# Kernel tuning notes

Measured on AMD Instinct MI355X. Metric: run time of the kernel, lower is better.

Reference implementation:

```python
import jax, jax.numpy as jnp
import numpy as np

ALPHA = 0.5  # trapezoidal_alpha

def rmsnorm(x, w, eps=1e-5):
    return x * jax.lax.rsqrt(jnp.mean(x * x, axis=-1, keepdims=True) + eps) * w

def ssd_scan(x, Bc, Cc, dt, A, alpha):
    # x: (B,L,H,P), Bc/Cc: (B,L,N), dt: (B,L,H), A: (H,)
    da = jnp.exp(dt * A)  # (B,L,H), A < 0 so da in (0,1)
    shift = lambda t: jnp.concatenate([jnp.zeros_like(t[:, :1]), t[:, :-1]], axis=1)
    xp, bp, dtp = shift(x), shift(Bc), shift(dt)
    to_t = lambda t: jnp.moveaxis(t, 1, 0)
    xs = tuple(map(to_t, (x, Bc, Cc, dt, da, xp, bp, dtp)))
    Bb, _, H, P = x.shape
    N = Bc.shape[-1]
    h0 = jnp.zeros((Bb, H, P, N), x.dtype)
    def step(h, inp):
        xt, bt, ct, dtt, dat, xpt, bpt, dtpt = inp
        u = dtt[:, :, None, None] * xt[..., None] * bt[:, None, None, :]      # (B,H,P,N)
        up = dtpt[:, :, None, None] * xpt[..., None] * bpt[:, None, None, :]  # prev input term
        h = dat[:, :, None, None] * (h + alpha * up) + (1.0 - alpha) * u      # trapezoidal update
        y = jnp.einsum('bhpn,bn->bhp', h, ct)
        return h, y
    _, ys = jax.lax.scan(step, h0, xs)
    return jnp.moveaxis(ys, 0, 1)  # (B,L,H,P)

def setup_inputs() -> dict:
    key = jax.random.key(0)
    ks = jax.random.split(key, 10)
    B, NV, NQ = 4, 256, 32
    D, DI, H, N, E, NL = 1024, 2048, 32, 128, 1536, 12
    PROJ = 2 * DI + 2 * N + H  # z | x | B | C | dt
    s = 0.02
    return {
        'visual_tokens': jax.random.normal(ks[0], (B, NV, D), jnp.float32),
        'query_embeds': jax.random.normal(ks[1], (B, NQ, D), jnp.float32),
        'vis_w': jax.random.normal(ks[2], (D, D), jnp.float32) * s,
        'vis_b': jnp.zeros((D,), jnp.float32),
        'qry_w': jax.random.normal(ks[3], (D, D), jnp.float32) * s,
        'qry_b': jnp.zeros((D,), jnp.float32),
        'norm_ws': jnp.ones((NL, D), jnp.float32),
        'in_ws': jax.random.normal(ks[4], (NL, D, PROJ), jnp.float32) * s,
        'dt_biases': jax.random.normal(ks[5], (NL, H), jnp.float32) * 0.5,
        'A_logs': jnp.log(jnp.tile(jnp.arange(1.0, H + 1.0, dtype=jnp.float32)[None], (NL, 1))),
        'D_ssm': jnp.ones((NL, H), jnp.float32),
        'gnorm_ws': jnp.ones((NL, DI), jnp.float32),
        'out_ws': jax.random.normal(ks[6], (NL, DI, D), jnp.float32) * s,
        'norm_f_w': jnp.ones((D,), jnp.float32),
        'head_w': jax.random.normal(ks[7], (D, E), jnp.float32) * s,
        'head_b': jnp.zeros((E,), jnp.float32),
    }

def reference(visual_tokens, query_embeds, vis_w, vis_b, qry_w, qry_b, norm_ws, in_ws,
              dt_biases, A_logs, D_ssm, gnorm_ws, out_ws, norm_f_w, head_w, head_b):
    vis = visual_tokens @ vis_w + vis_b
    qry = query_embeds @ qry_w + qry_b
    hidden = jnp.concatenate([vis, qry], axis=1)  # (B,L,D)
    n_layers = in_ws.shape[0]
    d_inner = gnorm_ws.shape[-1]
    H = A_logs.shape[-1]
    P = d_inner // H
    N = (in_ws.shape[-1] - 2 * d_inner - H) // 2
    for i in range(n_layers):
        res = hidden
        xin = rmsnorm(hidden, norm_ws[i])
        proj = xin @ in_ws[i]  # (B,L,2*DI+2*N+H)
        z = proj[..., :d_inner]
        xss = proj[..., d_inner:2 * d_inner]
        Bc = proj[..., 2 * d_inner:2 * d_inner + N]
        Cc = proj[..., 2 * d_inner + N:2 * d_inner + 2 * N]
        dt = jax.nn.softplus(proj[..., 2 * d_inner + 2 * N:] + dt_biases[i])
        A = -jnp.exp(A_logs[i])
        xr = xss.reshape(xss.shape[0], xss.shape[1], H, P)
        y = ssd_scan(xr, Bc, Cc, dt, A, ALPHA) + D_ssm[i][None, None, :, None] * xr
        y = y.reshape(xss.shape)
        y = rmsnorm(y * jax.nn.silu(z), gnorm_ws[i])  # gated RMSNorm
        hidden = res + y @ out_ws[i]
    hidden = rmsnorm(hidden, norm_f_w)
    pooled = hidden.mean(axis=1)                   # (B,D)
    out = pooled @ head_w + head_b                 # (B,E)
    nrm = jnp.linalg.norm(out, axis=-1, keepdims=True)
    return out / jnp.maximum(nrm, 1e-12)           # F.normalize semantics
```

## Files before the change

kernel.cpp:

```cpp
#include <hip/hip_runtime.h>
#include <cmath>

#define Bb   4
#define Tt   288
#define Dd   1024
#define DIi  2048
#define HH   32
#define PP   64
#define NNs  128
#define PROJ  4384
#define PROJP 4480
#define NLl  12
#define EE   1536

typedef __bf16 bf16x8 __attribute__((ext_vector_type(8)));
typedef float f32x4 __attribute__((ext_vector_type(4)));
typedef float f32x16 __attribute__((ext_vector_type(16)));

__device__ __forceinline__ unsigned short f2bf(float v) {
  __bf16 b = (__bf16)v;
  return __builtin_bit_cast(unsigned short, b);
}
__device__ __forceinline__ float bf2f(unsigned short u) {
  unsigned int x = ((unsigned int)u) << 16;
  return __builtin_bit_cast(float, x);
}
__device__ __forceinline__ void split2(float v, unsigned short& h, unsigned short& l) {
  h = f2bf(v);
  l = f2bf(v - bf2f(h));
}

__device__ __forceinline__ void async16(const void* g, void* l) {
  __builtin_amdgcn_global_load_lds(
      (const __attribute__((address_space(1))) unsigned int*)g,
      (__attribute__((address_space(3))) unsigned int*)l, 16, 0, 0);
}

__device__ inline float block_reduce_sum(float v, float* lds) {
#pragma unroll
  for (int d = 32; d > 0; d >>= 1) v += __shfl_down(v, d, 64);
  int lane = threadIdx.x & 63;
  int w = threadIdx.x >> 6;
  if (lane == 0) lds[w] = v;
  __syncthreads();
  if (threadIdx.x == 0) {
    float s = lds[0];
    int nw = blockDim.x >> 6;
    for (int i = 1; i < nw; i++) s += lds[i];
    lds[0] = s;
  }
  __syncthreads();
  return lds[0];
}

__global__ __launch_bounds__(256) void cvt_act_k(const float* __restrict__ vis,
                                                 const float* __restrict__ qry,
                                                 unsigned short* __restrict__ oh,
                                                 unsigned short* __restrict__ ol) {
  int idx = (blockIdx.x * 256 + threadIdx.x) * 4;
  const float* src = (idx < 1024 * 1024) ? &vis[idx] : &qry[idx - 1024 * 1024];
  float4 v = *(const float4*)src;
  ushort4 h, l;
  split2(v.x, h.x, l.x); split2(v.y, h.y, l.y);
  split2(v.z, h.z, l.z); split2(v.w, h.w, l.w);
  *(ushort4*)&oh[idx] = h;
  *(ushort4*)&ol[idx] = l;
}

__global__ __launch_bounds__(256) void cvt_tr2_k(const float* __restrict__ W,
                                                 unsigned short* __restrict__ Wth,
                                                 unsigned short* __restrict__ Wtl,
                                                 int K, int N,
                                                 size_t wstride, size_t ostride) {
  __shared__ float tile[32][33];
  W   += (size_t)blockIdx.z * wstride;
  Wth += (size_t)blockIdx.z * ostride;
  Wtl += (size_t)blockIdx.z * ostride;
  const int n0 = blockIdx.x * 32, k0 = blockIdx.y * 32;
  const int c = threadIdx.x & 31;
  const int r0 = threadIdx.x >> 5;
#pragma unroll
  for (int j = 0; j < 4; j++) {
    int r = r0 + j * 8;
    int n = n0 + c;
    tile[r][c] = (n < N) ? W[(size_t)(k0 + r) * N + n] : 0.f;
  }
  __syncthreads();
  const int nl = threadIdx.x >> 3;
  const int kl = (threadIdx.x & 7) * 4;
  ushort4 h, l;
  split2(tile[kl + 0][nl], h.x, l.x);
  split2(tile[kl + 1][nl], h.y, l.y);
  split2(tile[kl + 2][nl], h.z, l.z);
  split2(tile[kl + 3][nl], h.w, l.w);
  size_t o = (size_t)(n0 + nl) * K + k0 + kl;
  *(ushort4*)&Wth[o] = h;
  *(ushort4*)&Wtl[o] = l;
}

template<int BM, int BN>
__global__ __launch_bounds__(256) void gemm3_k(
    const unsigned short* __restrict__ Ah, const unsigned short* __restrict__ Al,
    const unsigned short* __restrict__ Wh, const unsigned short* __restrict__ Wl,
    const float* __restrict__ bias, const float* __restrict__ res,
    float* __restrict__ C, int M, int N, int K,
    int rows_per_b, int T_total, int t_off)
{
  constexpr int FM = BM / 64;
  constexpr int FN = BN / 64;
  __shared__ __align__(16) unsigned short Ash[BM * 32];
  __shared__ __align__(16) unsigned short Asl[BM * 32];
  __shared__ __align__(16) unsigned short Bsh[BN * 32];
  __shared__ __align__(16) unsigned short Bsl[BN * 32];
  const int tid = threadIdx.x;
  const int lane = tid & 63;
  const int wm = (tid >> 6) >> 1;
  const int wn = (tid >> 6) & 1;
  const int m0 = blockIdx.y * BM;
  const int n0 = blockIdx.x * BN;
  const int lrow = lane & 31;
  const int lkb = (lane >> 5) * 8;

  f32x16 acc[FM][FN];
#pragma unroll
  for (int i = 0; i < FM; i++)
#pragma unroll
    for (int j = 0; j < FN; j++) acc[i][j] = (f32x16)0.0f;

  for (int k0 = 0; k0 < K; k0 += 32) {
#pragma unroll
    for (int c = 0; c < BM / 64; c++) {
      int o = (c * 256 + tid) * 16;
      int row = o >> 6;
      int colb = o & 63;
      size_t gb = ((size_t)(m0 + row) * K + k0) * 2 + colb;
      async16((const char*)Ah + gb, (char*)Ash + o);
      async16((const char*)Al + gb, (char*)Asl + o);
    }
#pragma unroll
    for (int c = 0; c < BN / 64; c++) {
      int o = (c * 256 + tid) * 16;
      int row = o >> 6;
      int colb = o & 63;
      size_t gb = ((size_t)(n0 + row) * K + k0) * 2 + colb;
      async16((const char*)Wh + gb, (char*)Bsh + o);
      async16((const char*)Wl + gb, (char*)Bsl + o);
    }
    __syncthreads();

#pragma unroll
    for (int kh = 0; kh < 2; kh++) {
      bf16x8 ah[FM], al[FM], bh[FN], bl[FN];
#pragma unroll
      for (int i = 0; i < FM; i++) {
        int off = (wm * (BM / 2) + i * 32 + lrow) * 32 + kh * 16 + lkb;
        ah[i] = *(const bf16x8*)&Ash[off];
        al[i] = *(const bf16x8*)&Asl[off];
      }
#pragma unroll
      for (int j = 0; j < FN; j++) {
        int off = (wn * (BN / 2) + j * 32 + lrow) * 32 + kh * 16 + lkb;
        bh[j] = *(const bf16x8*)&Bsh[off];
        bl[j] = *(const bf16x8*)&Bsl[off];
      }
#pragma unroll
      for (int i = 0; i < FM; i++)
#pragma unroll
        for (int j = 0; j < FN; j++) {
          acc[i][j] = __builtin_amdgcn_mfma_f32_32x32x16_bf16(ah[i], bh[j], acc[i][j], 0, 0, 0);
          acc[i][j] = __builtin_amdgcn_mfma_f32_32x32x16_bf16(ah[i], bl[j], acc[i][j], 0, 0, 0);
          acc[i][j] = __builtin_amdgcn_mfma_f32_32x32x16_bf16(al[i], bh[j], acc[i][j], 0, 0, 0);
        }
    }
    __syncthreads();
  }

  const int r0 = (lane >> 5) * 4;
#pragma unroll
  for (int i = 0; i < FM; i++) {
#pragma unroll
    for (int j = 0; j < FN; j++) {
      int ncol = n0 + wn * (BN / 2) + j * 32 + lrow;
      float bv = bias ? bias[ncol] : 0.f;
#pragma unroll
      for (int rg = 0; rg < 16; rg++) {
        int m = m0 + wm * (BM / 2) + i * 32 + (rg & 3) + 8 * (rg >> 2) + r0;
        size_t orow;
        if (T_total) {
          int bbv = m / rows_per_b;
          orow = (size_t)bbv * T_total + (m - bbv * rows_per_b) + t_off;
        } else {
          orow = (size_t)m;
        }
        float v = acc[i][j][rg] + bv;
        if (res) v += res[orow * N + ncol];
        C[orow * N + ncol] = v;
      }
    }
  }
}

__global__ __launch_bounds__(256) void gemm_k(
    const float* __restrict__ A, const float* __restrict__ W,
    const float* __restrict__ bias, const float* __restrict__ res,
    float* __restrict__ C, int M, int N, int K,
    int rows_per_b, int T_total, int t_off)
{
  __shared__ float As[16][64];
  __shared__ float Ws[16][64];
  const int tid = threadIdx.x;
  const int tx = tid & 15;
  const int ty = tid >> 4;
  const int m0 = blockIdx.y * 64;
  const int n0 = blockIdx.x * 64;
  float acc[4][4] = {};
  const int ar = tid >> 2;
  const int ac = (tid & 3) << 2;
  const int wr = tid >> 4;
  const int wc = (tid & 15) << 2;

  for (int k0 = 0; k0 < K; k0 += 16) {
    float4 av = {0.f, 0.f, 0.f, 0.f};
    int gr = m0 + ar;
    if (gr < M) av = *(const float4*)&A[(size_t)gr * K + k0 + ac];
    As[ac + 0][ar] = av.x; As[ac + 1][ar] = av.y;
    As[ac + 2][ar] = av.z; As[ac + 3][ar] = av.w;

    float4 wv = {0.f, 0.f, 0.f, 0.f};
    int gc = n0 + wc;
    const float* wp = &W[(size_t)(k0 + wr) * N + gc];
    if (gc + 3 < N) {
      wv = *(const float4*)wp;
    } else {
      if (gc + 0 < N) wv.x = wp[0];
      if (gc + 1 < N) wv.y = wp[1];
      if (gc + 2 < N) wv.z = wp[2];
    }
    *(float4*)&Ws[wr][wc] = wv;
    __syncthreads();
#pragma unroll
    for (int kk = 0; kk < 16; kk++) {
      float4 a4 = *(const float4*)&As[kk][ty << 2];
      float4 b4 = *(const float4*)&Ws[kk][tx << 2];
      float a[4] = {a4.x, a4.y, a4.z, a4.w};
      float b[4] = {b4.x, b4.y, b4.z, b4.w};
#pragma unroll
      for (int i = 0; i < 4; i++)
#pragma unroll
        for (int j = 0; j < 4; j++)
          acc[i][j] = fmaf(a[i], b[j], acc[i][j]);
    }
    __syncthreads();
  }
#pragma unroll
  for (int i = 0; i < 4; i++) {
    int gr = m0 + (ty << 2) + i;
    if (gr >= M) continue;
    int bbv = gr / rows_per_b;
    int tt = gr - bbv * rows_per_b;
    size_t orow = (size_t)bbv * T_total + tt + t_off;
#pragma unroll
    for (int j = 0; j < 4; j++) {
      int gc = n0 + (tx << 2) + j;
      if (gc >= N) continue;
      float v = acc[i][j];
      if (bias) v += bias[gc];
      if (res)  v += res[orow * (size_t)N + gc];
      C[orow * (size_t)N + gc] = v;
    }
  }
}

__global__ __launch_bounds__(256) void rmsnorm_k(
    const float* __restrict__ x, const float* __restrict__ w, float* __restrict__ out)
{
  __shared__ float lds[8];
  const int row = blockIdx.x;
  const float* xr = x + (size_t)row * Dd;
  float4 v = *(const float4*)&xr[threadIdx.x << 2];
  float ss = v.x * v.x + v.y * v.y + v.z * v.z + v.w * v.w;
  ss = block_reduce_sum(ss, lds);
  float sc = rsqrtf(ss * (1.f / Dd) + 1e-5f);
  float4 wv = *(const float4*)&w[threadIdx.x << 2];
  float4 o = {v.x * sc * wv.x, v.y * sc * wv.y, v.z * sc * wv.z, v.w * sc * wv.w};
  *(float4*)&out[(size_t)row * Dd + (threadIdx.x << 2)] = o;
}

__global__ __launch_bounds__(256) void rmsnorm2_k(
    const float* __restrict__ x, const float* __restrict__ w,
    unsigned short* __restrict__ oh, unsigned short* __restrict__ ol)
{
  __shared__ float lds[8];
  const int row = blockIdx.x;
  const float* xr = x + (size_t)row * Dd;
  float4 v = *(const float4*)&xr[threadIdx.x << 2];
  float ss = v.x * v.x + v.y * v.y + v.z * v.z + v.w * v.w;
  ss = block_reduce_sum(ss, lds);
  float sc = rsqrtf(ss * (1.f / Dd) + 1e-5f);
  float4 wv = *(const float4*)&w[threadIdx.x << 2];
  ushort4 h, l;
  split2(v.x * sc * wv.x, h.x, l.x);
  split2(v.y * sc * wv.y, h.y, l.y);
  split2(v.z * sc * wv.z, h.z, l.z);
  split2(v.w * sc * wv.w, h.w, l.w);
  size_t o = (size_t)row * Dd + (threadIdx.x << 2);
  *(ushort4*)&oh[o] = h;
  *(ushort4*)&ol[o] = l;
}

__global__ __launch_bounds__(64) void dtcum_k(
    const float* __restrict__ proj, const float* __restrict__ dt_bias,
    const float* __restrict__ A_log,
    float* __restrict__ dtt, double* __restrict__ dcum)
{
  const int h = blockIdx.x & 31;
  const int b = blockIdx.x >> 5;
  const int lane = threadIdx.x;
  const float A = -expf(A_log[h]);
  const float bias = dt_bias[h];
  const int rowo = (b * HH + h) * Tt;
  double base = 0.0;
  for (int c = 0; c < (Tt + 63) / 64; c++) {
    int t = c * 64 + lane;
    float dt = 0.f;
    if (t < Tt) {
      float v = proj[(size_t)(b * Tt + t) * PROJP + 2 * DIi + 2 * NNs + h] + bias;
      dt = (v > 20.f) ? v : log1pf(expf(v));
    }
    double a = (double)(dt * A);
#pragma unroll
    for (int d = 1; d < 64; d <<= 1) {
      double o = __shfl_up(a, d, 64);
      if (lane >= d) a += o;
    }
    double cum = base + a;
    if (t < Tt) { dtt[rowo + t] = dt; dcum[rowo + t] = cum; }
    base = __shfl(cum, 63, 64);
  }
}

__global__ __launch_bounds__(256) void cbgemm_k(const float* __restrict__ proj,
                                                float* __restrict__ St)
{
  const int tI = blockIdx.x, jI = blockIdx.y, b = blockIdx.z;
  if (jI > tI) return;
  __shared__ float Ct[32][130];
  __shared__ float Bt[32][130];
  const int tid = threadIdx.x;
  const int r = tid >> 3;
  const int q = (tid & 7) * 16;
  const float* pb = proj + (size_t)b * Tt * PROJP;
  {
    const float* crow = pb + (size_t)(tI * 32 + r) * PROJP + 2 * DIi + NNs + q;
    const float* brow = pb + (size_t)(jI * 32 + r) * PROJP + 2 * DIi + q;
#pragma unroll
    for (int f = 0; f < 16; f += 4) {
      float4 c4 = *(const float4*)&crow[f];
      float4 b4 = *(const float4*)&brow[f];
      *(float2*)&Ct[r][q + f]     = make_float2(c4.x, c4.y);
      *(float2*)&Ct[r][q + f + 2] = make_float2(c4.z, c4.w);
      *(float2*)&Bt[r][q + f]     = make_float2(b4.x, b4.y);
      *(float2*)&Bt[r][q + f + 2] = make_float2(b4.z, b4.w);
    }
  }
  __syncthreads();
  const int j_r = tid >> 3;
  const int t_c = (tid & 7) * 4;
  float acc[4] = {0.f, 0.f, 0.f, 0.f};
  for (int n = 0; n < NNs; n += 2) {
    float2 b2 = *(const float2*)&Bt[j_r][n];
#pragma unroll
    for (int k = 0; k < 4; k++) {
      float2 c2 = *(const float2*)&Ct[t_c + k][n];
      acc[k] = fmaf(b2.x, c2.x, acc[k]);
      acc[k] = fmaf(b2.y, c2.y, acc[k]);
    }
  }
  float* so = St + ((size_t)b * Tt + jI * 32 + j_r) * Tt + tI * 32 + t_c;
  *(float4*)so = make_float4(acc[0], acc[1], acc[2], acc[3]);
}

__global__ __launch_bounds__(256) void ssd_y_k(
    const float* __restrict__ proj, const float* __restrict__ St,
    const float* __restrict__ dtt, const double* __restrict__ dcum,
    const float* __restrict__ Dssm, float* __restrict__ ybuf)
{
  const int tI = blockIdx.x;
  const int h  = blockIdx.y;
  const int b  = blockIdx.z;
  __shared__ __align__(16) float Xs[32][64];
  __shared__ __align__(16) float Ss[32][36];
  __shared__ double cjs[32];
  const int tid = threadIdx.x;
  const int t_l = tid & 31;
  const int pg  = tid >> 5;
  const int t0  = tI * 32;
  const int rowo = (b * HH + h) * Tt;
  const double ct = dcum[rowo + t0 + t_l];
  const float Ds = Dssm[h];
  const float* pb = proj + (size_t)b * Tt * PROJP;
  float y[8] = {0,0,0,0,0,0,0,0};
  const int sr = tid >> 3;
  const int sq = tid & 7;

  for (int jI = 0; jI <= tI; jI++) {
    const int j0 = jI * 32;
    {
      const float* xr = pb + (size_t)(j0 + sr) * PROJP + DIi + h * PP + sq * 8;
      *(float4*)&Xs[sr][sq * 8]     = *(const float4*)&xr[0];
      *(float4*)&Xs[sr][sq * 8 + 4] = *(const float4*)&xr[4];
    }
    {
      const float* srow = St + ((size_t)b * Tt + j0 + sr) * Tt + t0 + sq * 4;
      float4 s4 = *(const float4*)srow;
      float dj = dtt[rowo + j0 + sr];
      s4.x *= dj; s4.y *= dj; s4.z *= dj; s4.w *= dj;
      *(float4*)&Ss[sr][sq * 4] = s4;
    }
    if (tid < 32) cjs[tid] = dcum[rowo + j0 + tid];
    __syncthreads();

    if (jI < tI) {
#pragma unroll 4
      for (int j = 0; j < 32; j++) {
        float d = (float)(ct - cjs[j]);
        float m = Ss[j][t_l] * expf(fminf(d, 0.f));
        const float* xp = &Xs[j][pg * 8];
        float4 a0 = *(const float4*)&xp[0];
        float4 a1 = *(const float4*)&xp[4];
        y[0] = fmaf(m, a0.x, y[0]); y[1] = fmaf(m, a0.y, y[1]);
        y[2] = fmaf(m, a0.z, y[2]); y[3] = fmaf(m, a0.w, y[3]);
        y[4] = fmaf(m, a1.x, y[4]); y[5] = fmaf(m, a1.y, y[5]);
        y[6] = fmaf(m, a1.z, y[6]); y[7] = fmaf(m, a1.w, y[7]);
      }
    } else {
      for (int j = 0; j < 32; j++) {
        float sv = Ss[j][t_l];
        float d = (float)(ct - cjs[j]);
        float m = sv * expf(fminf(d, 0.f));
        if (j == t_l) m = 0.5f * sv + Ds;
        if (j > t_l)  m = 0.f;
        const float* xp = &Xs[j][pg * 8];
        float4 a0 = *(const float4*)&xp[0];
        float4 a1 = *(const float4*)&xp[4];
        y[0] = fmaf(m, a0.x, y[0]); y[1] = fmaf(m, a0.y, y[1]);
        y[2] = fmaf(m, a0.z, y[2]); y[3] = fmaf(m, a0.w, y[3]);
        y[4] = fmaf(m, a1.x, y[4]); y[5] = fmaf(m, a1.y, y[5]);
        y[6] = fmaf(m, a1.z, y[6]); y[7] = fmaf(m, a1.w, y[7]);
      }
    }
    __syncthreads();
  }
  float* yo = &ybuf[(size_t)(b * Tt + t0 + t_l) * DIi + h * PP + pg * 8];
  *(float4*)&yo[0] = make_float4(y[0], y[1], y[2], y[3]);
  *(float4*)&yo[4] = make_float4(y[4], y[5], y[6], y[7]);
}

__global__ __launch_bounds__(256) void gate_norm2_k(
    const float* __restrict__ ybuf, const float* __restrict__ proj,
    const float* __restrict__ gw,
    unsigned short* __restrict__ yh, unsigned short* __restrict__ yl)
{
  __shared__ float lds[8];
  const int row = blockIdx.x;
  const float* yr = ybuf + (size_t)row * DIi;
  const float* zr = proj + (size_t)row * PROJP;
  const int base = threadIdx.x << 3;
  float4 z0 = *(const float4*)&zr[base];
  float4 z1 = *(const float4*)&zr[base + 4];
  float4 y0 = *(const float4*)&yr[base];
  float4 y1 = *(const float4*)&yr[base + 4];
  float zz[8] = {z0.x, z0.y, z0.z, z0.w, z1.x, z1.y, z1.z, z1.w};
  float yy[8] = {y0.x, y0.y, y0.z, y0.w, y1.x, y1.y, y1.z, y1.w};
  float g[8];
  float ss = 0.f;
#pragma unroll
  for (int e = 0; e < 8; e++) {
    float s = zz[e] / (1.f + expf(-zz[e]));
    float gv = yy[e] * s;
    g[e] = gv;
    ss += gv * gv;
  }
  ss = block_reduce_sum(ss, lds);
  float sc = rsqrtf(ss * (1.f / DIi) + 1e-5f);
  ushort4 h0, l0, h1, l1;
  split2(g[0] * sc * gw[base + 0], h0.x, l0.x);
  split2(g[1] * sc * gw[base + 1], h0.y, l0.y);
  split2(g[2] * sc * gw[base + 2], h0.z, l0.z);
  split2(g[3] * sc * gw[base + 3], h0.w, l0.w);
  split2(g[4] * sc * gw[base + 4], h1.x, l1.x);
  split2(g[5] * sc * gw[base + 5], h1.y, l1.y);
  split2(g[6] * sc * gw[base + 6], h1.z, l1.z);
  split2(g[7] * sc * gw[base + 7], h1.w, l1.w);
  size_t o = (size_t)row * DIi + base;
  *(ushort4*)&yh[o] = h0; *(ushort4*)&yh[o + 4] = h1;
  *(ushort4*)&yl[o] = l0; *(ushort4*)&yl[o + 4] = l1;
}

__global__ void pool_k(const float* __restrict__ xin, float* __restrict__ pooled) {
  int b = blockIdx.x;
  int d = blockIdx.y * 256 + threadIdx.x;
  const float* base = xin + (size_t)b * Tt * Dd + d;
  float s = 0.f;
  for (int t = 0; t < Tt; t++) s += base[(size_t)t * Dd];
  pooled[b * Dd + d] = s * (1.f / Tt);
}

__global__ __launch_bounds__(256) void l2norm_k(float* __restrict__ out) {
  __shared__ float lds[8];
  const int row = blockIdx.x;
  float* r = out + (size_t)row * EE;
  float v[6];
  float ss = 0.f;
#pragma unroll
  for (int e = 0; e < 6; e++) {
    v[e] = r[(e << 8) + threadIdx.x];
    ss += v[e] * v[e];
  }
  ss = block_reduce_sum(ss, lds);
  float sc = 1.f / fmaxf(sqrtf(ss), 1e-12f);
#pragma unroll
  for (int e = 0; e < 6; e++) r[(e << 8) + threadIdx.x] = v[e] * sc;
}

extern "C" void kernel_launch(void* const* d_in, const int* in_sizes, int n_in,
                              void* d_out, int out_size, void* d_ws, size_t ws_size,
                              hipStream_t stream) {
  (void)in_sizes; (void)n_in; (void)out_size;
  const float* visual   = (const float*)d_in[0];
  const float* query    = (const float*)d_in[1];
  const float* vis_w    = (const float*)d_in[2];
  const float* vis_b    = (const float*)d_in[3];
  const float* qry_w    = (const float*)d_in[4];
  const float* qry_b    = (const float*)d_in[5];
  const float* norm_ws  = (const float*)d_in[6];
  const float* in_ws    = (const float*)d_in[7];
  const float* dt_biases= (const float*)d_in[8];
  const float* A_logs   = (const float*)d_in[9];
  const float* D_ssm    = (const float*)d_in[10];
  const float* gnorm_ws = (const float*)d_in[11];
  const float* out_ws   = (const float*)d_in[12];
  const float* norm_f_w = (const float*)d_in[13];
  const float* head_w   = (const float*)d_in[14];
  const float* head_b   = (const float*)d_in[15];
  float* out = (float*)d_out;

  char* w = (char*)d_ws;
  float*          hidden = (float*)w;          w += (size_t)1152 * 1024 * 4;
  unsigned short* xh     = (unsigned short*)w; w += (size_t)1152 * 1024 * 2;
  unsigned short* xl     = (unsigned short*)w; w += (size_t)1152 * 1024 * 2;
  float*          proj   = (float*)w;          w += (size_t)1152 * PROJP * 4;
  float*          ybuf   = (float*)w;          w += (size_t)1152 * 2048 * 4;
  unsigned short* yh     = (unsigned short*)w; w += (size_t)1152 * 2048 * 2;
  unsigned short* yl     = (unsigned short*)w; w += (size_t)1152 * 2048 * 2;
  float*          dtt    = (float*)w;          w += (size_t)Bb * HH * Tt * 4;
  double*         dcum   = (double*)w;         w += (size_t)Bb * HH * Tt * 8;
  float*          Stb    = (float*)w;          w += (size_t)Bb * Tt * Tt * 4;
  float*          pooled = (float*)w;          w += (size_t)4096 * 4;
  unsigned short* wth    = (unsigned short*)w; w += (size_t)PROJP * 1024 * 2;
  unsigned short* wtl    = (unsigned short*)w; w += (size_t)PROJP * 1024 * 2;

  unsigned short* wtin_h  = (unsigned short*)w; w += (size_t)NLl * PROJP * 1024 * 2;
  unsigned short* wtin_l  = (unsigned short*)w; w += (size_t)NLl * PROJP * 1024 * 2;
  unsigned short* wtout_h = (unsigned short*)w; w += (size_t)NLl * 1024 * 2048 * 2;
  unsigned short* wtout_l = (unsigned short*)w; w += (size_t)NLl * 1024 * 2048 * 2;
  unsigned short* wtv_h   = (unsigned short*)w; w += (size_t)1024 * 1024 * 2;
  unsigned short* wtv_l   = (unsigned short*)w; w += (size_t)1024 * 1024 * 2;
  unsigned short* wtq_h   = (unsigned short*)w; w += (size_t)1024 * 1024 * 2;
  unsigned short* wtq_l   = (unsigned short*)w; w += (size_t)1024 * 1024 * 2;
  const bool batched = ((size_t)(w - (char*)d_ws)) <= ws_size;

  dim3 blk(256);

  cvt_act_k<<<1152, blk, 0, stream>>>(visual, query, xh, xl);

  if (batched) {
    cvt_tr2_k<<<dim3(32, 32, 1), blk, 0, stream>>>(vis_w, wtv_h, wtv_l, 1024, 1024, 0, 0);
    cvt_tr2_k<<<dim3(32, 32, 1), blk, 0, stream>>>(qry_w, wtq_h, wtq_l, 1024, 1024, 0, 0);
    cvt_tr2_k<<<dim3(PROJP / 32, 32, NLl), blk, 0, stream>>>(
        in_ws, wtin_h, wtin_l, Dd, PROJ, (size_t)Dd * PROJ, (size_t)PROJP * 1024);
    cvt_tr2_k<<<dim3(32, 64, NLl), blk, 0, stream>>>(
        out_ws, wtout_h, wtout_l, DIi, Dd, (size_t)DIi * Dd, (size_t)1024 * 2048);
    gemm3_k<64, 64><<<dim3(16, 16), blk, 0, stream>>>(
        xh, xl, wtv_h, wtv_l, vis_b, nullptr, hidden, 1024, 1024, 1024, 256, Tt, 0);
    gemm3_k<64, 64><<<dim3(16, 2), blk, 0, stream>>>(
        xh + (size_t)1024 * 1024, xl + (size_t)1024 * 1024, wtq_h, wtq_l,
        qry_b, nullptr, hidden, 128, 1024, 1024, 32, Tt, 256);
  } else {
    cvt_tr2_k<<<dim3(32, 32, 1), blk, 0, stream>>>(vis_w, wth, wtl, 1024, 1024, 0, 0);
    gemm3_k<64, 64><<<dim3(16, 16), blk, 0, stream>>>(
        xh, xl, wth, wtl, vis_b, nullptr, hidden, 1024, 1024, 1024, 256, Tt, 0);
    cvt_tr2_k<<<dim3(32, 32, 1), blk, 0, stream>>>(qry_w, wth, wtl, 1024, 1024, 0, 0);
    gemm3_k<64, 64><<<dim3(16, 2), blk, 0, stream>>>(
        xh + (size_t)1024 * 1024, xl + (size_t)1024 * 1024, wth, wtl,
        qry_b, nullptr, hidden, 128, 1024, 1024, 32, Tt, 256);
  }

  for (int i = 0; i < NLl; i++) {
    rmsnorm2_k<<<Bb * Tt, blk, 0, stream>>>(hidden, norm_ws + i * Dd, xh, xl);
    const unsigned short *bih, *bil;
    if (batched) {
      bih = wtin_h + (size_t)i * PROJP * 1024;
      bil = wtin_l + (size_t)i * PROJP * 1024;
    } else {
      cvt_tr2_k<<<dim3(PROJP / 32, 32, 1), blk, 0, stream>>>(
          in_ws + (size_t)i * Dd * PROJ, wth, wtl, Dd, PROJ, 0, 0);
      bih = wth; bil = wtl;
    }
    gemm3_k<128, 128><<<dim3(PROJP / 128, 9), blk, 0, stream>>>(
        xh, xl, bih, bil, nullptr, nullptr, proj, 1152, PROJP, Dd, 1152, 0, 0);
    dtcum_k<<<Bb * HH, dim3(64), 0, stream>>>(proj, dt_biases + i * HH,
                                              A_logs + i * HH, dtt, dcum);
    cbgemm_k<<<dim3(9, 9, Bb), blk, 0, stream>>>(proj, Stb);
    ssd_y_k<<<dim3(9, HH, Bb), blk, 0, stream>>>(proj, Stb, dtt, dcum,
                                                 D_ssm + i * HH, ybuf);
    gate_norm2_k<<<Bb * Tt, blk, 0, stream>>>(ybuf, proj, gnorm_ws + i * DIi, yh, yl);
    const unsigned short *boh, *bol;
    if (batched) {
      boh = wtout_h + (size_t)i * 1024 * 2048;
      bol = wtout_l + (size_t)i * 1024 * 2048;
    } else {
      cvt_tr2_k<<<dim3(32, 64, 1), blk, 0, stream>>>(
          out_ws + (size_t)i * DIi * Dd, wth, wtl, DIi, Dd, 0, 0);
      boh = wth; bol = wtl;
    }
    gemm3_k<64, 64><<<dim3(16, 18), blk, 0, stream>>>(
        yh, yl, boh, bol, nullptr, hidden, hidden, 1152, Dd, DIi, 1152, 0, 0);
  }

  rmsnorm_k<<<Bb * Tt, blk, 0, stream>>>(hidden, norm_f_w, ybuf);
  pool_k<<<dim3(Bb, 4), blk, 0, stream>>>(ybuf, pooled);
  gemm_k<<<dim3(24, 1), blk, 0, stream>>>(pooled, head_w, head_b, nullptr, out,
                                          Bb, EE, Dd, Bb, 0, 0);
  l2norm_k<<<Bb, blk, 0, stream>>>(out);
}
```

Measured before the change: 2.935 ms.

## Switch GEMM to 16x16x32 MFMA, widen conversion kernels, fuse dt-cumsum with CB GEMM

```diff
diff --git a/kernel.cpp b/kernel.cpp
--- a/kernel.cpp
+++ b/kernel.cpp
@@ -15,7 +15,7 @@
 
 typedef __bf16 bf16x8 __attribute__((ext_vector_type(8)));
 typedef float f32x4 __attribute__((ext_vector_type(4)));
-typedef float f32x16 __attribute__((ext_vector_type(16)));
+typedef unsigned short ushort8 __attribute__((ext_vector_type(8)));
 
 __device__ __forceinline__ unsigned short f2bf(float v) {
   __bf16 b = (__bf16)v;
@@ -57,14 +57,17 @@
                                                  const float* __restrict__ qry,
                                                  unsigned short* __restrict__ oh,
                                                  unsigned short* __restrict__ ol) {
-  int idx = (blockIdx.x * 256 + threadIdx.x) * 4;
+  int idx = (blockIdx.x * 256 + threadIdx.x) * 8;
   const float* src = (idx < 1024 * 1024) ? &vis[idx] : &qry[idx - 1024 * 1024];
-  float4 v = *(const float4*)src;
-  ushort4 h, l;
-  split2(v.x, h.x, l.x); split2(v.y, h.y, l.y);
-  split2(v.z, h.z, l.z); split2(v.w, h.w, l.w);
-  *(ushort4*)&oh[idx] = h;
-  *(ushort4*)&ol[idx] = l;
+  float4 v0 = *(const float4*)&src[0];
+  float4 v1 = *(const float4*)&src[4];
+  unsigned short h[8], l[8];
+  split2(v0.x, h[0], l[0]); split2(v0.y, h[1], l[1]);
+  split2(v0.z, h[2], l[2]); split2(v0.w, h[3], l[3]);
+  split2(v1.x, h[4], l[4]); split2(v1.y, h[5], l[5]);
+  split2(v1.z, h[6], l[6]); split2(v1.w, h[7], l[7]);
+  *(ushort8*)&oh[idx] = *(const ushort8*)h;
+  *(ushort8*)&ol[idx] = *(const ushort8*)l;
 }
 
 __global__ __launch_bounds__(256) void cvt_tr2_k(const float* __restrict__ W,
@@ -72,30 +75,28 @@
                                                  unsigned short* __restrict__ Wtl,
                                                  int K, int N,
                                                  size_t wstride, size_t ostride) {
-  __shared__ float tile[32][33];
+  __shared__ float tile[64][33];
   W   += (size_t)blockIdx.z * wstride;
   Wth += (size_t)blockIdx.z * ostride;
   Wtl += (size_t)blockIdx.z * ostride;
-  const int n0 = blockIdx.x * 32, k0 = blockIdx.y * 32;
+  const int n0 = blockIdx.x * 32, k0 = blockIdx.y * 64;
   const int c = threadIdx.x & 31;
   const int r0 = threadIdx.x >> 5;
 #pragma unroll
-  for (int j = 0; j < 4; j++) {
+  for (int j = 0; j < 8; j++) {
     int r = r0 + j * 8;
     int n = n0 + c;
     tile[r][c] = (n < N) ? W[(size_t)(k0 + r) * N + n] : 0.f;
   }
   __syncthreads();
   const int nl = threadIdx.x >> 3;
-  const int kl = (threadIdx.x & 7) * 4;
-  ushort4 h, l;
-  split2(tile[kl + 0][nl], h.x, l.x);
-  split2(tile[kl + 1][nl], h.y, l.y);
-  split2(tile[kl + 2][nl], h.z, l.z);
-  split2(tile[kl + 3][nl], h.w, l.w);
-  size_t o = (size_t)(n0 + nl) * K + k0 + kl;
-  *(ushort4*)&Wth[o] = h;
-  *(ushort4*)&Wtl[o] = l;
+  const int kg = threadIdx.x & 7;
+  unsigned short h[8], l[8];
+#pragma unroll
+  for (int j = 0; j < 8; j++) split2(tile[kg * 8 + j][nl], h[j], l[j]);
+  size_t o = (size_t)(n0 + nl) * K + k0 + kg * 8;
+  *(ushort8*)&Wth[o] = *(const ushort8*)h;
+  *(ushort8*)&Wtl[o] = *(const ushort8*)l;
 }
 
 template<int BM, int BN>
@@ -106,8 +107,8 @@
     float* __restrict__ C, int M, int N, int K,
     int rows_per_b, int T_total, int t_off)
 {
-  constexpr int FM = BM / 64;
-  constexpr int FN = BN / 64;
+  constexpr int FM = BM / 32;
+  constexpr int FN = BN / 32;
   __shared__ __align__(16) unsigned short Ash[BM * 32];
   __shared__ __align__(16) unsigned short Asl[BM * 32];
   __shared__ __align__(16) unsigned short Bsh[BN * 32];
@@ -118,14 +119,14 @@
   const int wn = (tid >> 6) & 1;
   const int m0 = blockIdx.y * BM;
   const int n0 = blockIdx.x * BN;
-  const int lrow = lane & 31;
-  const int lkb = (lane >> 5) * 8;
-
-  f32x16 acc[FM][FN];
+  const int lrow = lane & 15;
+  const int lkb = (lane >> 4) * 8;
+
+  f32x4 acc[FM][FN];
 #pragma unroll
   for (int i = 0; i < FM; i++)
 #pragma unroll
-    for (int j = 0; j < FN; j++) acc[i][j] = (f32x16)0.0f;
+    for (int j = 0; j < FN; j++) acc[i][j] = (f32x4)0.0f;
 
   for (int k0 = 0; k0 < K; k0 += 32) {
 #pragma unroll
@@ -148,43 +149,41 @@
     }
     __syncthreads();
 
-#pragma unroll
-    for (int kh = 0; kh < 2; kh++) {
-      bf16x8 ah[FM], al[FM], bh[FN], bl[FN];
-#pragma unroll
-      for (int i = 0; i < FM; i++) {
-        int off = (wm * (BM / 2) + i * 32 + lrow) * 32 + kh * 16 + lkb;
-        ah[i] = *(const bf16x8*)&Ash[off];
-        al[i] = *(const bf16x8*)&Asl[off];
+    bf16x8 ah[FM], al[FM], bh[FN], bl[FN];
+#pragma unroll
+    for (int i = 0; i < FM; i++) {
+      int off = (wm * (FM * 16) + i * 16 + lrow) * 32 + lkb;
+      ah[i] = *(const bf16x8*)&Ash[off];
+      al[i] = *(const bf16x8*)&Asl[off];
+    }
+#pragma unroll
+    for (int j = 0; j < FN; j++) {
+      int off = (wn * (FN * 16) + j * 16 + lrow) * 32 + lkb;
+      bh[j] = *(const bf16x8*)&Bsh[off];
+      bl[j] = *(const bf16x8*)&Bsl[off];
+    }
+#pragma unroll
+    for (int i = 0; i < FM; i++)
+#pragma unroll
+      for (int j = 0; j < FN; j++) {
+        acc[i][j] = __builtin_amdgcn_mfma_f32_16x16x32_bf16(ah[i], bh[j], acc[i][j], 0, 0, 0);
+        acc[i][j] = __builtin_amdgcn_mfma_f32_16x16x32_bf16(ah[i], bl[j], acc[i][j], 0, 0, 0);
+        acc[i][j] = __builtin_amdgcn_mfma_f32_16x16x32_bf16(al[i], bh[j], acc[i][j], 0, 0, 0);
       }
-#pragma unroll
-      for (int j = 0; j < FN; j++) {
-        int off = (wn * (BN / 2) + j * 32 + lrow) * 32 + kh * 16 + lkb;
-        bh[j] = *(const bf16x8*)&Bsh[off];
-        bl[j] = *(const bf16x8*)&Bsl[off];
-      }
-#pragma unroll
-      for (int i = 0; i < FM; i++)
-#pragma unroll
-        for (int j = 0; j < FN; j++) {
-          acc[i][j] = __builtin_amdgcn_mfma_f32_32x32x16_bf16(ah[i], bh[j], acc[i][j], 0, 0, 0);
-          acc[i][j] = __builtin_amdgcn_mfma_f32_32x32x16_bf16(ah[i], bl[j], acc[i][j], 0, 0, 0);
-          acc[i][j] = __builtin_amdgcn_mfma_f32_32x32x16_bf16(al[i], bh[j], acc[i][j], 0, 0, 0);
-        }
-    }
     __syncthreads();
   }
 
-  const int r0 = (lane >> 5) * 4;
+  const int erow = (lane >> 4) * 4;
 #pragma unroll
   for (int i = 0; i < FM; i++) {
+    int mbase = m0 + wm * (FM * 16) + i * 16 + erow;
 #pragma unroll
     for (int j = 0; j < FN; j++) {
-      int ncol = n0 + wn * (BN / 2) + j * 32 + lrow;
+      int ncol = n0 + wn * (FN * 16) + j * 16 + lrow;
       float bv = bias ? bias[ncol] : 0.f;
 #pragma unroll
-      for (int rg = 0; rg < 16; rg++) {
-        int m = m0 + wm * (BM / 2) + i * 32 + (rg & 3) + 8 * (rg >> 2) + r0;
+      for (int e = 0; e < 4; e++) {
+        int m = mbase + e;
         size_t orow;
         if (T_total) {
           int bbv = m / rows_per_b;
@@ -192,7 +191,7 @@
         } else {
           orow = (size_t)m;
         }
-        float v = acc[i][j][rg] + bv;
+        float v = acc[i][j][e] + bv;
         if (res) v += res[orow * N + ncol];
         C[orow * N + ncol] = v;
       }
@@ -308,44 +307,46 @@
   *(ushort4*)&ol[o] = l;
 }
 
-__global__ __launch_bounds__(64) void dtcum_k(
-    const float* __restrict__ proj, const float* __restrict__ dt_bias,
-    const float* __restrict__ A_log,
-    float* __restrict__ dtt, double* __restrict__ dcum)
+__global__ __launch_bounds__(256) void sscb_k(const float* __restrict__ proj,
+                                              const float* __restrict__ dt_bias,
+                                              const float* __restrict__ A_log,
+                                              float* __restrict__ dtt,
+                                              double* __restrict__ dcum,
+                                              float* __restrict__ St)
 {
-  const int h = blockIdx.x & 31;
-  const int b = blockIdx.x >> 5;
-  const int lane = threadIdx.x;
-  const float A = -expf(A_log[h]);
-  const float bias = dt_bias[h];
-  const int rowo = (b * HH + h) * Tt;
-  double base = 0.0;
-  for (int c = 0; c < (Tt + 63) / 64; c++) {
-    int t = c * 64 + lane;
-    float dt = 0.f;
-    if (t < Tt) {
-      float v = proj[(size_t)(b * Tt + t) * PROJP + 2 * DIi + 2 * NNs + h] + bias;
-      dt = (v > 20.f) ? v : log1pf(expf(v));
-    }
-    double a = (double)(dt * A);
-#pragma unroll
-    for (int d = 1; d < 64; d <<= 1) {
-      double o = __shfl_up(a, d, 64);
-      if (lane >= d) a += o;
-    }
-    double cum = base + a;
-    if (t < Tt) { dtt[rowo + t] = dt; dcum[rowo + t] = cum; }
-    base = __shfl(cum, 63, 64);
-  }
-}
-
-__global__ __launch_bounds__(256) void cbgemm_k(const float* __restrict__ proj,
-                                                float* __restrict__ St)
-{
+  __shared__ float Ct[32][130];
+  __shared__ float Bt[32][130];
+  if (blockIdx.y == 9) {
+    if (blockIdx.x >= 8) return;
+    const int wv = threadIdx.x >> 6;
+    const int lane = threadIdx.x & 63;
+    const int h = blockIdx.x * 4 + wv;
+    const int b = blockIdx.z;
+    const float A = -expf(A_log[h]);
+    const float bias = dt_bias[h];
+    const int rowo = (b * HH + h) * Tt;
+    double base = 0.0;
+    for (int c = 0; c < (Tt + 63) / 64; c++) {
+      int t = c * 64 + lane;
+      float dt = 0.f;
+      if (t < Tt) {
+        float v = proj[(size_t)(b * Tt + t) * PROJP + 2 * DIi + 2 * NNs + h] + bias;
+        dt = (v > 20.f) ? v : log1pf(expf(v));
+      }
+      double a = (double)(dt * A);
+#pragma unroll
+      for (int d = 1; d < 64; d <<= 1) {
+        double o = __shfl_up(a, d, 64);
+        if (lane >= d) a += o;
+      }
+      double cum = base + a;
+      if (t < Tt) { dtt[rowo + t] = dt; dcum[rowo + t] = cum; }
+      base = __shfl(cum, 63, 64);
+    }
+    return;
+  }
   const int tI = blockIdx.x, jI = blockIdx.y, b = blockIdx.z;
   if (jI > tI) return;
-  __shared__ float Ct[32][130];
-  __shared__ float Bt[32][130];
   const int tid = threadIdx.x;
   const int r = tid >> 3;
   const int q = (tid & 7) * 16;
@@ -483,18 +484,12 @@
   }
   ss = block_reduce_sum(ss, lds);
   float sc = rsqrtf(ss * (1.f / DIi) + 1e-5f);
-  ushort4 h0, l0, h1, l1;
-  split2(g[0] * sc * gw[base + 0], h0.x, l0.x);
-  split2(g[1] * sc * gw[base + 1], h0.y, l0.y);
-  split2(g[2] * sc * gw[base + 2], h0.z, l0.z);
-  split2(g[3] * sc * gw[base + 3], h0.w, l0.w);
-  split2(g[4] * sc * gw[base + 4], h1.x, l1.x);
-  split2(g[5] * sc * gw[base + 5], h1.y, l1.y);
-  split2(g[6] * sc * gw[base + 6], h1.z, l1.z);
-  split2(g[7] * sc * gw[base + 7], h1.w, l1.w);
+  unsigned short h[8], l[8];
+#pragma unroll
+  for (int e = 0; e < 8; e++) split2(g[e] * sc * gw[base + e], h[e], l[e]);
   size_t o = (size_t)row * DIi + base;
-  *(ushort4*)&yh[o] = h0; *(ushort4*)&yh[o + 4] = h1;
-  *(ushort4*)&yl[o] = l0; *(ushort4*)&yl[o + 4] = l1;
+  *(ushort8*)&yh[o] = *(const ushort8*)h;
+  *(ushort8*)&yl[o] = *(const ushort8*)l;
 }
 
 __global__ void pool_k(const float* __restrict__ xin, float* __restrict__ pooled) {
@@ -572,14 +567,14 @@
 
   dim3 blk(256);
 
-  cvt_act_k<<<1152, blk, 0, stream>>>(visual, query, xh, xl);
+  cvt_act_k<<<576, blk, 0, stream>>>(visual, query, xh, xl);
 
   if (batched) {
-    cvt_tr2_k<<<dim3(32, 32, 1), blk, 0, stream>>>(vis_w, wtv_h, wtv_l, 1024, 1024, 0, 0);
-    cvt_tr2_k<<<dim3(32, 32, 1), blk, 0, stream>>>(qry_w, wtq_h, wtq_l, 1024, 1024, 0, 0);
-    cvt_tr2_k<<<dim3(PROJP / 32, 32, NLl), blk, 0, stream>>>(
+    cvt_tr2_k<<<dim3(32, 16, 1), blk, 0, stream>>>(vis_w, wtv_h, wtv_l, 1024, 1024, 0, 0);
+    cvt_tr2_k<<<dim3(32, 16, 1), blk, 0, stream>>>(qry_w, wtq_h, wtq_l, 1024, 1024, 0, 0);
+    cvt_tr2_k<<<dim3(PROJP / 32, 16, NLl), blk, 0, stream>>>(
         in_ws, wtin_h, wtin_l, Dd, PROJ, (size_t)Dd * PROJ, (size_t)PROJP * 1024);
-    cvt_tr2_k<<<dim3(32, 64, NLl), blk, 0, stream>>>(
+    cvt_tr2_k<<<dim3(32, 32, NLl), blk, 0, stream>>>(
         out_ws, wtout_h, wtout_l, DIi, Dd, (size_t)DIi * Dd, (size_t)1024 * 2048);
     gemm3_k<64, 64><<<dim3(16, 16), blk, 0, stream>>>(
         xh, xl, wtv_h, wtv_l, vis_b, nullptr, hidden, 1024, 1024, 1024, 256, Tt, 0);
@@ -587,10 +582,10 @@
         xh + (size_t)1024 * 1024, xl + (size_t)1024 * 1024, wtq_h, wtq_l,
         qry_b, nullptr, hidden, 128, 1024, 1024, 32, Tt, 256);
   } else {
-    cvt_tr2_k<<<dim3(32, 32, 1), blk, 0, stream>>>(vis_w, wth, wtl, 1024, 1024, 0, 0);
+    cvt_tr2_k<<<dim3(32, 16, 1), blk, 0, stream>>>(vis_w, wth, wtl, 1024, 1024, 0, 0);
     gemm3_k<64, 64><<<dim3(16, 16), blk, 0, stream>>>(
         xh, xl, wth, wtl, vis_b, nullptr, hidden, 1024, 1024, 1024, 256, Tt, 0);
-    cvt_tr2_k<<<dim3(32, 32, 1), blk, 0, stream>>>(qry_w, wth, wtl, 1024, 1024, 0, 0);
+    cvt_tr2_k<<<dim3(32, 16, 1), blk, 0, stream>>>(qry_w, wth, wtl, 1024, 1024, 0, 0);
     gemm3_k<64, 64><<<dim3(16, 2), blk, 0, stream>>>(
         xh + (size_t)1024 * 1024, xl + (size_t)1024 * 1024, wth, wtl,
         qry_b, nullptr, hidden, 128, 1024, 1024, 32, Tt, 256);
@@ -603,15 +598,14 @@
       bih = wtin_h + (size_t)i * PROJP * 1024;
       bil = wtin_l + (size_t)i * PROJP * 1024;
     } else {
-      cvt_tr2_k<<<dim3(PROJP / 32, 32, 1), blk, 0, stream>>>(
+      cvt_tr2_k<<<dim3(PROJP / 32, 16, 1), blk, 0, stream>>>(
           in_ws + (size_t)i * Dd * PROJ, wth, wtl, Dd, PROJ, 0, 0);
       bih = wth; bil = wtl;
     }
     gemm3_k<128, 128><<<dim3(PROJP / 128, 9), blk, 0, stream>>>(
         xh, xl, bih, bil, nullptr, nullptr, proj, 1152, PROJP, Dd, 1152, 0, 0);
-    dtcum_k<<<Bb * HH, dim3(64), 0, stream>>>(proj, dt_biases + i * HH,
-                                              A_logs + i * HH, dtt, dcum);
-    cbgemm_k<<<dim3(9, 9, Bb), blk, 0, stream>>>(proj, Stb);
+    sscb_k<<<dim3(9, 10, Bb), blk, 0, stream>>>(proj, dt_biases + i * HH,
+                                                A_logs + i * HH, dtt, dcum, Stb);
     ssd_y_k<<<dim3(9, HH, Bb), blk, 0, stream>>>(proj, Stb, dtt, dcum,
                                                  D_ssm + i * HH, ybuf);
     gate_norm2_k<<<Bb * Tt, blk, 0, stream>>>(ybuf, proj, gnorm_ws + i * DIi, yh, yl);
@@ -620,7 +614,7 @@
       boh = wtout_h + (size_t)i * 1024 * 2048;
       bol = wtout_l + (size_t)i * 1024 * 2048;
     } else {
-      cvt_tr2_k<<<dim3(32, 64, 1), blk, 0, stream>>>(
+      cvt_tr2_k<<<dim3(32, 32, 1), blk, 0, stream>>>(
           out_ws + (size_t)i * DIi * Dd, wth, wtl, DIi, Dd, 0, 0);
       boh = wth; bol = wtl;
     }
```

Result: faster. 2.738 ms (-6.7%).
